# Optimization experiments

Hardware: AMD Instinct MI355X
Metric: run time of the kernel (lower is better)

Reference implementation:

```python
import jax, jax.numpy as jnp
import numpy as np

VOCAB = 32000
E = 512      # embed_dim
H = 512      # hidden_dim (== embed_dim, required by the output-averaging slice)
NUM_LAYERS = 2
WIN = 8
S = 512      # seq_len
B = 8        # batch


def setup_inputs() -> dict:
    key = jax.random.key(0)
    ks = jax.random.split(key, 40)
    d = {"encoder_input": jax.random.randint(ks[0], (S, B), 0, VOCAB, dtype=jnp.int64
                                             if jax.config.jax_enable_x64 else jnp.int32)}
    d["embed_table"] = jax.random.normal(ks[1], (VOCAB, E), jnp.float32) * 0.02
    i = 2
    for l in range(NUM_LAYERS):
        in_dim = E if l == 0 else 2 * H
        for dirn in ("f", "b"):
            sc = 1.0 / np.sqrt(H).astype(np.float32)
            d[f"wih{l}{dirn}"] = jax.random.normal(ks[i], (4 * H, in_dim), jnp.float32) * sc; i += 1
            d[f"whh{l}{dirn}"] = jax.random.normal(ks[i], (4 * H, H), jnp.float32) * sc; i += 1
            d[f"b{l}{dirn}"] = jax.random.normal(ks[i], (4 * H,), jnp.float32) * sc; i += 1
    return d


def _lstm_dir(x, mask, wih, whh, b, reverse):
    """One LSTM direction over padded windows. x: [L, N, in], mask: [L, N, 1].
    Masked (out-of-window) steps carry state unchanged; since invalid steps form a
    prefix in scan order (left pad for fwd, right pad for bwd-reversed), the zero
    initial state is preserved until the first valid step -> identical math to
    running the LSTM on the truncated window, as in the original per-token loop."""
    Hh = whh.shape[1]

    def step(carry, inp):
        h, c = carry
        xt, mt = inp
        g = xt @ wih.T + h @ whh.T + b                      # [N, 4H], torch gate order i,f,g,o
        i_, f_, g_, o_ = jnp.split(g, 4, axis=-1)
        c_new = jax.nn.sigmoid(f_) * c + jax.nn.sigmoid(i_) * jnp.tanh(g_)
        h_new = jax.nn.sigmoid(o_) * jnp.tanh(c_new)
        h = jnp.where(mt, h_new, h)
        c = jnp.where(mt, c_new, c)
        return (h, c), h

    N = x.shape[1]
    h0 = jnp.zeros((N, Hh), x.dtype)
    _, ys = jax.lax.scan(step, (h0, h0), (x, mask), reverse=reverse)
    return ys  # [L, N, Hh]


def _forward(encoder_input, embed_table, layer_params):
    S_, B_ = encoder_input.shape
    L = 2 * WIN + 1
    emb = embed_table[encoder_input]                         # [S, B, E]
    offs = jnp.arange(L) - WIN
    pos = jnp.arange(S_)[:, None] + offs[None, :]            # [S, L]
    valid = (pos >= 0) & (pos < S_)
    pidx = jnp.clip(pos, 0, S_ - 1)
    windows = emb[pidx]                                      # [S, L, B, E]
    x = windows.transpose(1, 0, 2, 3).reshape(L, S_ * B_, E)  # [L, N, E]
    mask = jnp.broadcast_to(valid.T[:, :, None, None], (L, S_, B_, 1)).reshape(L, S_ * B_, 1)
    for (wf, hf, bf, wb, hb, bb) in layer_params:
        yf = _lstm_dir(x, mask, wf, hf, bf, reverse=False)
        yb = _lstm_dir(x, mask, wb, hb, bb, reverse=True)
        x = jnp.concatenate([yf, yb], axis=-1)               # [L, N, 2H]
    out = x[WIN].reshape(S_, B_, 2 * H)                      # [S, B, 2H]
    return (out[:, :, :E] + out[:, :, E:]) / 2


def reference(encoder_input, embed_table,
              wih0f, whh0f, b0f, wih0b, whh0b, b0b,
              wih1f, whh1f, b1f, wih1b, whh1b, b1b):
    layer_params = [(wih0f, whh0f, b0f, wih0b, whh0b, b0b),
                    (wih1f, whh1f, b1f, wih1b, whh1b, b1b)]
    return _forward(encoder_input, embed_table, layer_params)
```

## Files before the change

kernel.cpp:

```cpp
#include <hip/hip_runtime.h>
#include <stdint.h>

typedef __bf16 bf16;
typedef __bf16 bf16x8 __attribute__((ext_vector_type(8)));
typedef __bf16 bf16x4 __attribute__((ext_vector_type(4)));
typedef float f32x4 __attribute__((ext_vector_type(4)));

#define WIN 8

__device__ __forceinline__ float sigm(float x) { return 1.0f / (1.0f + __expf(-x)); }
__device__ __forceinline__ float tanhfast(float x) { return 2.0f / (1.0f + __expf(-2.0f * x)) - 1.0f; }

__device__ __forceinline__ void gload16(const void* g, void* l) {
    __builtin_amdgcn_global_load_lds((const __attribute__((address_space(1))) void*)g,
                                     (__attribute__((address_space(3))) void*)l, 16, 0, 0);
}

struct StepArgs {
    const bf16* A1;
    const bf16* A2;
    const bf16* W;
    const float* bias;
    const bf16* P0;
    float* Cst;
    bf16* Hout;
    float* Hf32;
    const bf16* Hprev;
    int l;
    int firstStep;
};

template<int MODE>
__global__ __launch_bounds__(512, 2)
void step_pair(StepArgs fa, StepArgs ba) {
    const StepArgs a = blockIdx.z ? ba : fa;
    __shared__ alignas(16) char lds[131072];

    constexpr int SA1 = (MODE == 0) ? 512 : 1024;
    constexpr int SW  = (MODE == 2) ? 1536 : 512;
    constexpr int SH  = (MODE == 0) ? 2048 : (MODE == 1 ? 1024 : 512);
    constexpr int SHP = (MODE == 1) ? 1024 : 512;

    const int tid = threadIdx.x;
    const int w = tid >> 6;
    const int lane = tid & 63;
    const int wm = w >> 2, wn = w & 3;
    const int bx = blockIdx.x, by = blockIdx.y;
    const int rowBase = bx * 256;

    int KB;
    if (MODE == 0) KB = 8;
    else if (MODE == 1) KB = a.firstStep ? 0 : 8;
    else KB = a.firstStep ? 16 : 24;

    const int lq = lane >> 3;
    const int lc = lane & 7;
    const int swz = 8 * (lc ^ lq);

    const bf16* aP[4];
    const bf16* a2P[4];
    const bf16* bP[4];
#pragma unroll
    for (int q = 0; q < 4; ++q) {
        const int r = w * 32 + q * 8 + lq;
        const int n = rowBase + r;
        aP[q] = a.A1 ? (a.A1 + (size_t)n * SA1 + swz) : (const bf16*)0;
        if (MODE == 2) a2P[q] = a.A2 ? (a.A2 + (size_t)n * 512 + swz) : (const bf16*)0;
        int wr;
        if (MODE == 0) wr = by * 256 + r;
        else wr = ((r & 63) >> 4) * 512 + by * 64 + (r >> 6) * 16 + (r & 15);
        bP[q] = a.W + (size_t)wr * SW + swz;
    }

    const int l15 = lane & 15, l4 = lane >> 4;
    const int key = (l15 & 7) << 4;
    const int aBase = (wm * 128 + l15) * 128;
    const int bBase = (wn * 64 + l15) * 128;

    f32x4 acc[8][4];
    const f32x4 zf = {0.f, 0.f, 0.f, 0.f};
#pragma unroll
    for (int m = 0; m < 8; ++m)
#pragma unroll
        for (int n = 0; n < 4; ++n) acc[m][n] = zf;

    auto CHUNK = [&](char* Sd, int kb, int q) {
        const int ke = kb * 64;
        const int ldsOff = (w * 32 + q * 8) * 128;
        const bf16* srcA;
        if (MODE == 2) srcA = (kb < 16) ? (aP[q] + ke) : (a2P[q] + (ke - 1024));
        else srcA = aP[q] + ke;
        gload16(srcA, Sd + ldsOff);
        gload16(bP[q] + ke, Sd + 32768 + ldsOff);
    };

    if (KB > 0) {
#pragma unroll
        for (int q = 0; q < 4; ++q) CHUNK(lds, 0, q);
        asm volatile("s_waitcnt vmcnt(0)" ::: "memory");
        __builtin_amdgcn_s_barrier();

        for (int t = 0; t < KB; ++t) {
            const int cur = t & 1;
            const char* Ab = lds + cur * 65536;
            const char* Bb = Ab + 32768;
            char* Sd = lds + (cur ^ 1) * 65536;
            const bool pf = (t + 1 < KB);
            const int ko0 = (l4 * 16) ^ key;
            const int ko1 = (64 + l4 * 16) ^ key;
            bf16x8 af0[4], af1[4], bv0[4], bv1[4];

            if (pf) { CHUNK(Sd, t + 1, 0); CHUNK(Sd, t + 1, 1); }
#pragma unroll
            for (int i = 0; i < 4; ++i)
                af0[i] = *(const bf16x8*)(Ab + aBase + i * 2048 + ko0);
#pragma unroll
            for (int n = 0; n < 4; ++n)
                bv0[n] = *(const bf16x8*)(Bb + bBase + n * 2048 + ko0);
            __builtin_amdgcn_s_barrier();
            asm volatile("s_waitcnt lgkmcnt(0)" ::: "memory");
            __builtin_amdgcn_sched_barrier(0);
            __builtin_amdgcn_s_setprio(1);
#pragma unroll
            for (int i = 0; i < 4; ++i)
#pragma unroll
                for (int n = 0; n < 4; ++n)
                    acc[i][n] = __builtin_amdgcn_mfma_f32_16x16x32_bf16(af0[i], bv0[n], acc[i][n], 0, 0, 0);
            __builtin_amdgcn_s_setprio(0);
            __builtin_amdgcn_sched_barrier(0);
            __builtin_amdgcn_s_barrier();

            if (pf) CHUNK(Sd, t + 1, 2);
#pragma unroll
            for (int i = 0; i < 4; ++i)
                af1[i] = *(const bf16x8*)(Ab + aBase + (4 + i) * 2048 + ko0);
            __builtin_amdgcn_s_barrier();
            asm volatile("s_waitcnt lgkmcnt(0)" ::: "memory");
            __builtin_amdgcn_sched_barrier(0);
            __builtin_amdgcn_s_setprio(1);
#pragma unroll
            for (int i = 0; i < 4; ++i)
#pragma unroll
                for (int n = 0; n < 4; ++n)
                    acc[4 + i][n] = __builtin_amdgcn_mfma_f32_16x16x32_bf16(af1[i], bv0[n], acc[4 + i][n], 0, 0, 0);
            __builtin_amdgcn_s_setprio(0);
            __builtin_amdgcn_sched_barrier(0);
            __builtin_amdgcn_s_barrier();

            if (pf) CHUNK(Sd, t + 1, 3);
#pragma unroll
            for (int i = 0; i < 4; ++i)
                af0[i] = *(const bf16x8*)(Ab + aBase + i * 2048 + ko1);
#pragma unroll
            for (int n = 0; n < 4; ++n)
                bv1[n] = *(const bf16x8*)(Bb + bBase + n * 2048 + ko1);
            __builtin_amdgcn_s_barrier();
            asm volatile("s_waitcnt lgkmcnt(0)" ::: "memory");
            __builtin_amdgcn_sched_barrier(0);
            __builtin_amdgcn_s_setprio(1);
#pragma unroll
            for (int i = 0; i < 4; ++i)
#pragma unroll
                for (int n = 0; n < 4; ++n)
                    acc[i][n] = __builtin_amdgcn_mfma_f32_16x16x32_bf16(af0[i], bv1[n], acc[i][n], 0, 0, 0);
            __builtin_amdgcn_s_setprio(0);
            __builtin_amdgcn_sched_barrier(0);
            __builtin_amdgcn_s_barrier();

#pragma unroll
            for (int i = 0; i < 4; ++i)
                af1[i] = *(const bf16x8*)(Ab + aBase + (4 + i) * 2048 + ko1);
            __builtin_amdgcn_s_barrier();
            asm volatile("s_waitcnt lgkmcnt(0)" ::: "memory");
            __builtin_amdgcn_sched_barrier(0);
            __builtin_amdgcn_s_setprio(1);
#pragma unroll
            for (int i = 0; i < 4; ++i)
#pragma unroll
                for (int n = 0; n < 4; ++n)
                    acc[4 + i][n] = __builtin_amdgcn_mfma_f32_16x16x32_bf16(af1[i], bv1[n], acc[4 + i][n], 0, 0, 0);
            __builtin_amdgcn_s_setprio(0);
            __builtin_amdgcn_sched_barrier(0);
            if (pf) asm volatile("s_waitcnt vmcnt(0)" ::: "memory");
            __builtin_amdgcn_s_barrier();
        }
    }

    if (MODE == 0) {
#pragma unroll
        for (int m = 0; m < 8; ++m)
#pragma unroll
            for (int n = 0; n < 4; ++n) {
                const int col = by * 256 + wn * 64 + n * 16 + l15;
#pragma unroll
                for (int e = 0; e < 4; ++e) {
                    const int row = rowBase + wm * 128 + m * 16 + l4 * 4 + e;
                    a.Hout[(size_t)row * SH + col] = (bf16)acc[m][n][e];
                }
            }
        return;
    }

    const int u = by * 64 + wn * 16 + l15;
    const float bi = a.bias[u];
    const float bff = a.bias[512 + u];
    const float bg = a.bias[1024 + u];
    const float bo = a.bias[1536 + u];
#pragma unroll
    for (int m = 0; m < 8; ++m) {
#pragma unroll
        for (int e = 0; e < 4; ++e) {
            const int n = rowBase + wm * 128 + m * 16 + l4 * 4 + e;
            const int s = n >> 3;
            const int p = s + a.l - WIN;
            const bool valid = ((unsigned)p < 512u);
            float gi = acc[m][0][e] + bi;
            float gf = acc[m][1][e] + bff;
            float gg = acc[m][2][e] + bg;
            float go = acc[m][3][e] + bo;
            if (MODE == 1) {
                const int pc = p < 0 ? 0 : (p > 511 ? 511 : p);
                const size_t pr = (size_t)(pc * 8 + (n & 7)) * 2048;
                gi += (float)a.P0[pr + u];
                gf += (float)a.P0[pr + 512 + u];
                gg += (float)a.P0[pr + 1024 + u];
                go += (float)a.P0[pr + 1536 + u];
            }
            const float cold = a.firstStep ? 0.0f : a.Cst[(size_t)n * 512 + u];
            const float cnew = sigm(gf) * cold + sigm(gi) * tanhfast(gg);
            const float hnew = sigm(go) * tanhfast(cnew);
            float hv, cv;
            if (valid) { hv = hnew; cv = cnew; }
            else {
                hv = a.Hprev ? (float)a.Hprev[(size_t)n * SHP + u] : 0.0f;
                cv = cold;
            }
            a.Cst[(size_t)n * 512 + u] = cv;
            a.Hout[(size_t)n * SH + u] = (bf16)hv;
            if (a.Hf32) a.Hf32[(size_t)n * 512 + u] = hv;
        }
    }
}

__global__ void embed_kernel(const int* __restrict__ tok, const float* __restrict__ tbl,
                             bf16* __restrict__ X0) {
    const int n = blockIdx.x;
    const int t = tok[n];
    const float4 v = ((const float4*)(tbl + (size_t)t * 512))[threadIdx.x];
    bf16x4 o = {(bf16)v.x, (bf16)v.y, (bf16)v.z, (bf16)v.w};
    ((bf16x4*)(X0 + (size_t)n * 512))[threadIdx.x] = o;
}

__global__ void cvt_kernel(const float* __restrict__ src, bf16* __restrict__ dst, int n4) {
    const int i = blockIdx.x * 256 + threadIdx.x;
    if (i < n4) {
        const float4 v = ((const float4*)src)[i];
        bf16x4 o = {(bf16)v.x, (bf16)v.y, (bf16)v.z, (bf16)v.w};
        ((bf16x4*)dst)[i] = o;
    }
}

__global__ void build_w1_kernel(const float* __restrict__ wih, const float* __restrict__ whh,
                                bf16* __restrict__ dst) {
    const int r = blockIdx.x;
    for (int k = threadIdx.x; k < 1536; k += 256) {
        const float v = (k < 1024) ? wih[(size_t)r * 1024 + k] : whh[(size_t)r * 512 + (k - 1024)];
        dst[(size_t)r * 1536 + k] = (bf16)v;
    }
}

__global__ void combine_kernel(const float* __restrict__ hf, const float* __restrict__ hb,
                               float* __restrict__ out) {
    const int i = blockIdx.x * 256 + threadIdx.x;
    const float4 x = ((const float4*)hf)[i];
    const float4 y = ((const float4*)hb)[i];
    float4 r;
    r.x = (x.x + y.x) * 0.5f;
    r.y = (x.y + y.y) * 0.5f;
    r.z = (x.z + y.z) * 0.5f;
    r.w = (x.w + y.w) * 0.5f;
    ((float4*)out)[i] = r;
}

extern "C" void kernel_launch(void* const* d_in, const int* in_sizes, int n_in,
                              void* d_out, int out_size, void* d_ws, size_t ws_size,
                              hipStream_t stream) {
    (void)in_sizes; (void)n_in; (void)out_size;
    const int*   tok   = (const int*)d_in[0];
    const float* tbl   = (const float*)d_in[1];
    const float* wih0f = (const float*)d_in[2];
    const float* whh0f = (const float*)d_in[3];
    const float* b0f   = (const float*)d_in[4];
    const float* wih0b = (const float*)d_in[5];
    const float* whh0b = (const float*)d_in[6];
    const float* b0b   = (const float*)d_in[7];
    const float* wih1f = (const float*)d_in[8];
    const float* whh1f = (const float*)d_in[9];
    const float* b1f   = (const float*)d_in[10];
    const float* wih1b = (const float*)d_in[11];
    const float* whh1b = (const float*)d_in[12];
    const float* b1b   = (const float*)d_in[13];

    char* ws = (char*)d_ws;
    size_t off = 0;
    auto alloc = [&](size_t bytes) -> char* {
        char* p = ws + off;
        off += (bytes + 255) & ~(size_t)255;
        return p;
    };
    bf16* wih0f_b = (bf16*)alloc((size_t)2048 * 512 * 2);
    bf16* wih0b_b = (bf16*)alloc((size_t)2048 * 512 * 2);
    bf16* whh0f_b = (bf16*)alloc((size_t)2048 * 512 * 2);
    bf16* whh0b_b = (bf16*)alloc((size_t)2048 * 512 * 2);
    bf16* w1f_b   = (bf16*)alloc((size_t)2048 * 1536 * 2);
    bf16* w1b_b   = (bf16*)alloc((size_t)2048 * 1536 * 2);
    bf16* X0      = (bf16*)alloc((size_t)4096 * 512 * 2);
    bf16* P0f     = (bf16*)alloc((size_t)4096 * 2048 * 2);
    bf16* P0b     = (bf16*)alloc((size_t)4096 * 2048 * 2);
    bf16* X1      = (bf16*)alloc((size_t)17 * 4096 * 1024 * 2);
    float* c0f    = (float*)alloc((size_t)4096 * 512 * 4);
    float* c0b    = (float*)alloc((size_t)4096 * 512 * 4);
    bf16* h1f0    = (bf16*)alloc((size_t)4096 * 512 * 2);
    bf16* h1f1    = (bf16*)alloc((size_t)4096 * 512 * 2);
    bf16* h1b0    = (bf16*)alloc((size_t)4096 * 512 * 2);
    bf16* h1b1    = (bf16*)alloc((size_t)4096 * 512 * 2);
    float* hf32f  = (float*)alloc((size_t)4096 * 512 * 4);
    float* hf32b  = (float*)alloc((size_t)4096 * 512 * 4);
    if (off > ws_size) return;

    bf16* h1f[2] = {h1f0, h1f1};
    bf16* h1b[2] = {h1b0, h1b1};

    cvt_kernel<<<1024, 256, 0, stream>>>(wih0f, wih0f_b, 262144);
    cvt_kernel<<<1024, 256, 0, stream>>>(wih0b, wih0b_b, 262144);
    cvt_kernel<<<1024, 256, 0, stream>>>(whh0f, whh0f_b, 262144);
    cvt_kernel<<<1024, 256, 0, stream>>>(whh0b, whh0b_b, 262144);
    build_w1_kernel<<<2048, 256, 0, stream>>>(wih1f, whh1f, w1f_b);
    build_w1_kernel<<<2048, 256, 0, stream>>>(wih1b, whh1b, w1b_b);
    embed_kernel<<<4096, 128, 0, stream>>>(tok, tbl, X0);

    dim3 g(16, 8, 2), blk(512, 1, 1);

    {
        StepArgs f{}, b{};
        f.A1 = X0; f.W = wih0f_b; f.Hout = P0f;
        b = f; b.W = wih0b_b; b.Hout = P0b;
        step_pair<0><<<g, blk, 0, stream>>>(f, b);
    }

    const size_t SLOT = (size_t)4096 * 1024;

    for (int i = 0; i <= 16; ++i) {
        const int lf = i, lb = 16 - i;
        StepArgs f{}, b{};
        f.A1 = (lf == 0) ? (const bf16*)0 : X1 + (size_t)(lf - 1) * SLOT;
        f.W = whh0f_b; f.bias = b0f; f.P0 = P0f; f.Cst = c0f;
        f.Hout = X1 + (size_t)lf * SLOT; f.Hprev = f.A1;
        f.l = lf; f.firstStep = (lf == 0) ? 1 : 0;
        b.A1 = (lb == 16) ? (const bf16*)0 : X1 + (size_t)(lb + 1) * SLOT + 512;
        b.W = whh0b_b; b.bias = b0b; b.P0 = P0b; b.Cst = c0b;
        b.Hout = X1 + (size_t)lb * SLOT + 512; b.Hprev = b.A1;
        b.l = lb; b.firstStep = (lb == 16) ? 1 : 0;
        step_pair<1><<<g, blk, 0, stream>>>(f, b);
    }

    for (int i = 0; i <= 8; ++i) {
        const int lf = i, lb = 16 - i;
        StepArgs f{}, b{};
        f.A1 = X1 + (size_t)lf * SLOT;
        f.A2 = (i == 0) ? (const bf16*)0 : h1f[(i + 1) & 1];
        f.W = w1f_b; f.bias = b1f; f.Cst = c0f;
        f.Hout = h1f[i & 1]; f.Hf32 = (i == 8) ? hf32f : (float*)0;
        f.Hprev = f.A2;
        f.l = lf; f.firstStep = (i == 0) ? 1 : 0;
        b.A1 = X1 + (size_t)lb * SLOT;
        b.A2 = (i == 0) ? (const bf16*)0 : h1b[(i + 1) & 1];
        b.W = w1b_b; b.bias = b1b; b.Cst = c0b;
        b.Hout = h1b[i & 1]; b.Hf32 = (i == 8) ? hf32b : (float*)0;
        b.Hprev = b.A2;
        b.l = lb; b.firstStep = (i == 0) ? 1 : 0;
        step_pair<2><<<g, blk, 0, stream>>>(f, b);
    }

    combine_kernel<<<2048, 256, 0, stream>>>(hf32f, hf32b, (float*)d_out);
}
```

Baseline: 1.089 ms.

## Fuse layer-0 input projection into each recurrent step GEMM via concatenated weights

Drops the precomputed layer-0 input projection (P0 GEMM over 4096 tokens) and instead concatenates W_hh and W_ih into one [2048,1024] weight, so each of the 17 layer-0 step kernels does an extra K=512 against shifted embedding rows. This removes the separate projection launch, the P0 buffers, and the scattered bf16 P0 gathers in the epilogue. In exchange it repeats the input projection 17 times, once per window slot, roughly doubling the MFMA work of the layer-0 steps.

```diff
diff --git a/kernel.cpp b/kernel.cpp
--- a/kernel.cpp
+++ b/kernel.cpp
@@ -21,7 +21,6 @@
     const bf16* A2;
     const bf16* W;
     const float* bias;
-    const bf16* P0;
     float* Cst;
     bf16* Hout;
     float* Hf32;
@@ -36,10 +35,12 @@
     const StepArgs a = blockIdx.z ? ba : fa;
     __shared__ alignas(16) char lds[131072];
 
-    constexpr int SA1 = (MODE == 0) ? 512 : 1024;
-    constexpr int SW  = (MODE == 2) ? 1536 : 512;
-    constexpr int SH  = (MODE == 0) ? 2048 : (MODE == 1 ? 1024 : 512);
+    constexpr int SA1 = 1024;
+    constexpr int SA2 = 512;
+    constexpr int SW  = (MODE == 2) ? 1536 : 1024;
+    constexpr int SH  = (MODE == 1) ? 1024 : 512;
     constexpr int SHP = (MODE == 1) ? 1024 : 512;
+    constexpr int ATILES = (MODE == 1) ? 8 : 16;
 
     const int tid = threadIdx.x;
     const int w = tid >> 6;
@@ -48,14 +49,14 @@
     const int bx = blockIdx.x, by = blockIdx.y;
     const int rowBase = bx * 256;
 
-    int KB;
-    if (MODE == 0) KB = 8;
-    else if (MODE == 1) KB = a.firstStep ? 0 : 8;
-    else KB = a.firstStep ? 16 : 24;
+    int KB, kt0;
+    if (MODE == 1) { KB = a.firstStep ? 8 : 16; kt0 = a.firstStep ? 8 : 0; }
+    else           { KB = a.firstStep ? 16 : 24; kt0 = 0; }
 
     const int lq = lane >> 3;
     const int lc = lane & 7;
     const int swz = 8 * (lc ^ lq);
+    const int d = (a.l - WIN) * 8;
 
     const bf16* aP[4];
     const bf16* a2P[4];
@@ -65,10 +66,14 @@
         const int r = w * 32 + q * 8 + lq;
         const int n = rowBase + r;
         aP[q] = a.A1 ? (a.A1 + (size_t)n * SA1 + swz) : (const bf16*)0;
-        if (MODE == 2) a2P[q] = a.A2 ? (a.A2 + (size_t)n * 512 + swz) : (const bf16*)0;
-        int wr;
-        if (MODE == 0) wr = by * 256 + r;
-        else wr = ((r & 63) >> 4) * 512 + by * 64 + (r >> 6) * 16 + (r & 15);
+        if (MODE == 1) {
+            int n2 = n + d;
+            n2 = n2 < 0 ? 0 : (n2 > 4095 ? 4095 : n2);
+            a2P[q] = a.A2 + (size_t)n2 * SA2 + swz;
+        } else {
+            a2P[q] = a.A2 ? (a.A2 + (size_t)n * SA2 + swz) : (const bf16*)0;
+        }
+        const int wr = ((r & 63) >> 4) * 512 + by * 64 + (r >> 6) * 16 + (r & 15);
         bP[q] = a.W + (size_t)wr * SW + swz;
     }
 
@@ -84,19 +89,18 @@
 #pragma unroll
         for (int n = 0; n < 4; ++n) acc[m][n] = zf;
 
-    auto CHUNK = [&](char* Sd, int kb, int q) {
-        const int ke = kb * 64;
+    auto CHUNK = [&](char* Sd, int kt, int q) {
         const int ldsOff = (w * 32 + q * 8) * 128;
         const bf16* srcA;
-        if (MODE == 2) srcA = (kb < 16) ? (aP[q] + ke) : (a2P[q] + (ke - 1024));
-        else srcA = aP[q] + ke;
+        if (kt < ATILES) srcA = aP[q] + kt * 64;
+        else srcA = a2P[q] + (kt - ATILES) * 64;
         gload16(srcA, Sd + ldsOff);
-        gload16(bP[q] + ke, Sd + 32768 + ldsOff);
+        gload16(bP[q] + (size_t)kt * 64, Sd + 32768 + ldsOff);
     };
 
-    if (KB > 0) {
-#pragma unroll
-        for (int q = 0; q < 4; ++q) CHUNK(lds, 0, q);
+    {
+#pragma unroll
+        for (int q = 0; q < 4; ++q) CHUNK(lds, kt0, q);
         asm volatile("s_waitcnt vmcnt(0)" ::: "memory");
         __builtin_amdgcn_s_barrier();
 
@@ -106,11 +110,12 @@
             const char* Bb = Ab + 32768;
             char* Sd = lds + (cur ^ 1) * 65536;
             const bool pf = (t + 1 < KB);
+            const int ktn = t + 1 + kt0;
             const int ko0 = (l4 * 16) ^ key;
             const int ko1 = (64 + l4 * 16) ^ key;
             bf16x8 af0[4], af1[4], bv0[4], bv1[4];
 
-            if (pf) { CHUNK(Sd, t + 1, 0); CHUNK(Sd, t + 1, 1); }
+            if (pf) { CHUNK(Sd, ktn, 0); CHUNK(Sd, ktn, 1); }
 #pragma unroll
             for (int i = 0; i < 4; ++i)
                 af0[i] = *(const bf16x8*)(Ab + aBase + i * 2048 + ko0);
@@ -130,7 +135,7 @@
             __builtin_amdgcn_sched_barrier(0);
             __builtin_amdgcn_s_barrier();
 
-            if (pf) CHUNK(Sd, t + 1, 2);
+            if (pf) CHUNK(Sd, ktn, 2);
 #pragma unroll
             for (int i = 0; i < 4; ++i)
                 af1[i] = *(const bf16x8*)(Ab + aBase + (4 + i) * 2048 + ko0);
@@ -147,7 +152,7 @@
             __builtin_amdgcn_sched_barrier(0);
             __builtin_amdgcn_s_barrier();
 
-            if (pf) CHUNK(Sd, t + 1, 3);
+            if (pf) CHUNK(Sd, ktn, 3);
 #pragma unroll
             for (int i = 0; i < 4; ++i)
                 af0[i] = *(const bf16x8*)(Ab + aBase + i * 2048 + ko1);
@@ -184,21 +189,6 @@
             if (pf) asm volatile("s_waitcnt vmcnt(0)" ::: "memory");
             __builtin_amdgcn_s_barrier();
         }
-    }
-
-    if (MODE == 0) {
-#pragma unroll
-        for (int m = 0; m < 8; ++m)
-#pragma unroll
-            for (int n = 0; n < 4; ++n) {
-                const int col = by * 256 + wn * 64 + n * 16 + l15;
-#pragma unroll
-                for (int e = 0; e < 4; ++e) {
-                    const int row = rowBase + wm * 128 + m * 16 + l4 * 4 + e;
-                    a.Hout[(size_t)row * SH + col] = (bf16)acc[m][n][e];
-                }
-            }
-        return;
     }
 
     const int u = by * 64 + wn * 16 + l15;
@@ -214,18 +204,10 @@
             const int s = n >> 3;
             const int p = s + a.l - WIN;
             const bool valid = ((unsigned)p < 512u);
-            float gi = acc[m][0][e] + bi;
-            float gf = acc[m][1][e] + bff;
-            float gg = acc[m][2][e] + bg;
-            float go = acc[m][3][e] + bo;
-            if (MODE == 1) {
-                const int pc = p < 0 ? 0 : (p > 511 ? 511 : p);
-                const size_t pr = (size_t)(pc * 8 + (n & 7)) * 2048;
-                gi += (float)a.P0[pr + u];
-                gf += (float)a.P0[pr + 512 + u];
-                gg += (float)a.P0[pr + 1024 + u];
-                go += (float)a.P0[pr + 1536 + u];
-            }
+            const float gi = acc[m][0][e] + bi;
+            const float gf = acc[m][1][e] + bff;
+            const float gg = acc[m][2][e] + bg;
+            const float go = acc[m][3][e] + bo;
             const float cold = a.firstStep ? 0.0f : a.Cst[(size_t)n * 512 + u];
             const float cnew = sigm(gf) * cold + sigm(gi) * tanhfast(gg);
             const float hnew = sigm(go) * tanhfast(cnew);
@@ -251,12 +233,12 @@
     ((bf16x4*)(X0 + (size_t)n * 512))[threadIdx.x] = o;
 }
 
-__global__ void cvt_kernel(const float* __restrict__ src, bf16* __restrict__ dst, int n4) {
-    const int i = blockIdx.x * 256 + threadIdx.x;
-    if (i < n4) {
-        const float4 v = ((const float4*)src)[i];
-        bf16x4 o = {(bf16)v.x, (bf16)v.y, (bf16)v.z, (bf16)v.w};
-        ((bf16x4*)dst)[i] = o;
+__global__ void build_w0_kernel(const float* __restrict__ wih, const float* __restrict__ whh,
+                                bf16* __restrict__ dst) {
+    const int r = blockIdx.x;
+    for (int k = threadIdx.x; k < 1024; k += 256) {
+        const float v = (k < 512) ? whh[(size_t)r * 512 + k] : wih[(size_t)r * 512 + (k - 512)];
+        dst[(size_t)r * 1024 + k] = (bf16)v;
     }
 }
 
@@ -308,15 +290,11 @@
         off += (bytes + 255) & ~(size_t)255;
         return p;
     };
-    bf16* wih0f_b = (bf16*)alloc((size_t)2048 * 512 * 2);
-    bf16* wih0b_b = (bf16*)alloc((size_t)2048 * 512 * 2);
-    bf16* whh0f_b = (bf16*)alloc((size_t)2048 * 512 * 2);
-    bf16* whh0b_b = (bf16*)alloc((size_t)2048 * 512 * 2);
+    bf16* w0f_b   = (bf16*)alloc((size_t)2048 * 1024 * 2);
+    bf16* w0b_b   = (bf16*)alloc((size_t)2048 * 1024 * 2);
     bf16* w1f_b   = (bf16*)alloc((size_t)2048 * 1536 * 2);
     bf16* w1b_b   = (bf16*)alloc((size_t)2048 * 1536 * 2);
     bf16* X0      = (bf16*)alloc((size_t)4096 * 512 * 2);
-    bf16* P0f     = (bf16*)alloc((size_t)4096 * 2048 * 2);
-    bf16* P0b     = (bf16*)alloc((size_t)4096 * 2048 * 2);
     bf16* X1      = (bf16*)alloc((size_t)17 * 4096 * 1024 * 2);
     float* c0f    = (float*)alloc((size_t)4096 * 512 * 4);
     float* c0b    = (float*)alloc((size_t)4096 * 512 * 4);
@@ -331,34 +309,26 @@
     bf16* h1f[2] = {h1f0, h1f1};
     bf16* h1b[2] = {h1b0, h1b1};
 
-    cvt_kernel<<<1024, 256, 0, stream>>>(wih0f, wih0f_b, 262144);
-    cvt_kernel<<<1024, 256, 0, stream>>>(wih0b, wih0b_b, 262144);
-    cvt_kernel<<<1024, 256, 0, stream>>>(whh0f, whh0f_b, 262144);
-    cvt_kernel<<<1024, 256, 0, stream>>>(whh0b, whh0b_b, 262144);
+    build_w0_kernel<<<2048, 256, 0, stream>>>(wih0f, whh0f, w0f_b);
+    build_w0_kernel<<<2048, 256, 0, stream>>>(wih0b, whh0b, w0b_b);
     build_w1_kernel<<<2048, 256, 0, stream>>>(wih1f, whh1f, w1f_b);
     build_w1_kernel<<<2048, 256, 0, stream>>>(wih1b, whh1b, w1b_b);
     embed_kernel<<<4096, 128, 0, stream>>>(tok, tbl, X0);
 
     dim3 g(16, 8, 2), blk(512, 1, 1);
-
-    {
-        StepArgs f{}, b{};
-        f.A1 = X0; f.W = wih0f_b; f.Hout = P0f;
-        b = f; b.W = wih0b_b; b.Hout = P0b;
-        step_pair<0><<<g, blk, 0, stream>>>(f, b);
-    }
-
     const size_t SLOT = (size_t)4096 * 1024;
 
     for (int i = 0; i <= 16; ++i) {
         const int lf = i, lb = 16 - i;
         StepArgs f{}, b{};
         f.A1 = (lf == 0) ? (const bf16*)0 : X1 + (size_t)(lf - 1) * SLOT;
-        f.W = whh0f_b; f.bias = b0f; f.P0 = P0f; f.Cst = c0f;
+        f.A2 = X0;
+        f.W = w0f_b; f.bias = b0f; f.Cst = c0f;
         f.Hout = X1 + (size_t)lf * SLOT; f.Hprev = f.A1;
         f.l = lf; f.firstStep = (lf == 0) ? 1 : 0;
         b.A1 = (lb == 16) ? (const bf16*)0 : X1 + (size_t)(lb + 1) * SLOT + 512;
-        b.W = whh0b_b; b.bias = b0b; b.P0 = P0b; b.Cst = c0b;
+        b.A2 = X0;
+        b.W = w0b_b; b.bias = b0b; b.Cst = c0b;
         b.Hout = X1 + (size_t)lb * SLOT + 512; b.Hprev = b.A1;
         b.l = lb; b.firstStep = (lb == 16) ? 1 : 0;
         step_pair<1><<<g, blk, 0, stream>>>(f, b);
```

After: 1.266 ms. 1.16x slower.

## Software-pipeline LDS fragment loads one phase ahead of MFMA in GEMM loop

Applied to the files above, without the earlier changes.

Restructures the inner K-loop so the LDS fragment reads for the next MFMA phase are issued before the current phase's MFMAs. Partial lgkmcnt waits replace full drains, so LDS reads overlap matrix math. The first fragments of the next K-block are preloaded from the freshly filled buffer at the end of each iteration. This adds register pressure from extra live fragment arrays, and it relies on the hand-counted lgkmcnt values being correct.

```diff
diff --git a/kernel.cpp b/kernel.cpp
--- a/kernel.cpp
+++ b/kernel.cpp
@@ -95,10 +95,20 @@
     };
 
     if (KB > 0) {
+        const int ko0 = (l4 * 16) ^ key;
+        const int ko1 = (64 + l4 * 16) ^ key;
+        bf16x8 afA[4], afB[4], bv0[4], bvp[4];
+
 #pragma unroll
         for (int q = 0; q < 4; ++q) CHUNK(lds, 0, q);
         asm volatile("s_waitcnt vmcnt(0)" ::: "memory");
         __builtin_amdgcn_s_barrier();
+#pragma unroll
+        for (int i = 0; i < 4; ++i)
+            afA[i] = *(const bf16x8*)(lds + aBase + i * 2048 + ko0);
+#pragma unroll
+        for (int n = 0; n < 4; ++n)
+            bv0[n] = *(const bf16x8*)(lds + 32768 + bBase + n * 2048 + ko0);
 
         for (int t = 0; t < KB; ++t) {
             const int cur = t & 1;
@@ -106,82 +116,82 @@
             const char* Bb = Ab + 32768;
             char* Sd = lds + (cur ^ 1) * 65536;
             const bool pf = (t + 1 < KB);
-            const int ko0 = (l4 * 16) ^ key;
-            const int ko1 = (64 + l4 * 16) ^ key;
-            bf16x8 af0[4], af1[4], bv0[4], bv1[4];
 
             if (pf) { CHUNK(Sd, t + 1, 0); CHUNK(Sd, t + 1, 1); }
 #pragma unroll
             for (int i = 0; i < 4; ++i)
-                af0[i] = *(const bf16x8*)(Ab + aBase + i * 2048 + ko0);
+                afB[i] = *(const bf16x8*)(Ab + aBase + (4 + i) * 2048 + ko0);
+            __builtin_amdgcn_s_barrier();
+            asm volatile("s_waitcnt lgkmcnt(4)" ::: "memory");
+            __builtin_amdgcn_sched_barrier(0);
+            __builtin_amdgcn_s_setprio(1);
+#pragma unroll
+            for (int i = 0; i < 4; ++i)
+#pragma unroll
+                for (int n = 0; n < 4; ++n)
+                    acc[i][n] = __builtin_amdgcn_mfma_f32_16x16x32_bf16(afA[i], bv0[n], acc[i][n], 0, 0, 0);
+            __builtin_amdgcn_s_setprio(0);
+            __builtin_amdgcn_sched_barrier(0);
+            __builtin_amdgcn_s_barrier();
+
+            if (pf) { CHUNK(Sd, t + 1, 2); CHUNK(Sd, t + 1, 3); }
+#pragma unroll
+            for (int i = 0; i < 4; ++i)
+                afA[i] = *(const bf16x8*)(Ab + aBase + i * 2048 + ko1);
 #pragma unroll
             for (int n = 0; n < 4; ++n)
-                bv0[n] = *(const bf16x8*)(Bb + bBase + n * 2048 + ko0);
-            __builtin_amdgcn_s_barrier();
-            asm volatile("s_waitcnt lgkmcnt(0)" ::: "memory");
+                bvp[n] = *(const bf16x8*)(Bb + bBase + n * 2048 + ko1);
+            __builtin_amdgcn_s_barrier();
+            asm volatile("s_waitcnt lgkmcnt(8)" ::: "memory");
             __builtin_amdgcn_sched_barrier(0);
             __builtin_amdgcn_s_setprio(1);
 #pragma unroll
             for (int i = 0; i < 4; ++i)
 #pragma unroll
                 for (int n = 0; n < 4; ++n)
-                    acc[i][n] = __builtin_amdgcn_mfma_f32_16x16x32_bf16(af0[i], bv0[n], acc[i][n], 0, 0, 0);
+                    acc[4 + i][n] = __builtin_amdgcn_mfma_f32_16x16x32_bf16(afB[i], bv0[n], acc[4 + i][n], 0, 0, 0);
             __builtin_amdgcn_s_setprio(0);
             __builtin_amdgcn_sched_barrier(0);
             __builtin_amdgcn_s_barrier();
 
-            if (pf) CHUNK(Sd, t + 1, 2);
-#pragma unroll
-            for (int i = 0; i < 4; ++i)
-                af1[i] = *(const bf16x8*)(Ab + aBase + (4 + i) * 2048 + ko0);
-            __builtin_amdgcn_s_barrier();
-            asm volatile("s_waitcnt lgkmcnt(0)" ::: "memory");
+#pragma unroll
+            for (int i = 0; i < 4; ++i)
+                afB[i] = *(const bf16x8*)(Ab + aBase + (4 + i) * 2048 + ko1);
+            __builtin_amdgcn_s_barrier();
+            asm volatile("s_waitcnt lgkmcnt(4)" ::: "memory");
             __builtin_amdgcn_sched_barrier(0);
             __builtin_amdgcn_s_setprio(1);
 #pragma unroll
             for (int i = 0; i < 4; ++i)
 #pragma unroll
                 for (int n = 0; n < 4; ++n)
-                    acc[4 + i][n] = __builtin_amdgcn_mfma_f32_16x16x32_bf16(af1[i], bv0[n], acc[4 + i][n], 0, 0, 0);
+                    acc[i][n] = __builtin_amdgcn_mfma_f32_16x16x32_bf16(afA[i], bvp[n], acc[i][n], 0, 0, 0);
             __builtin_amdgcn_s_setprio(0);
             __builtin_amdgcn_sched_barrier(0);
             __builtin_amdgcn_s_barrier();
 
-            if (pf) CHUNK(Sd, t + 1, 3);
-#pragma unroll
-            for (int i = 0; i < 4; ++i)
-                af0[i] = *(const bf16x8*)(Ab + aBase + i * 2048 + ko1);
-#pragma unroll
-            for (int n = 0; n < 4; ++n)
-                bv1[n] = *(const bf16x8*)(Bb + bBase + n * 2048 + ko1);
-            __builtin_amdgcn_s_barrier();
-            asm volatile("s_waitcnt lgkmcnt(0)" ::: "memory");
+            if (pf) asm volatile("s_waitcnt vmcnt(0)" ::: "memory");
+            __builtin_amdgcn_s_barrier();
+            if (pf) {
+#pragma unroll
+                for (int i = 0; i < 4; ++i)
+                    afA[i] = *(const bf16x8*)(Sd + aBase + i * 2048 + ko0);
+#pragma unroll
+                for (int n = 0; n < 4; ++n)
+                    bv0[n] = *(const bf16x8*)(Sd + 32768 + bBase + n * 2048 + ko0);
+                asm volatile("s_waitcnt lgkmcnt(8)" ::: "memory");
+            } else {
+                asm volatile("s_waitcnt lgkmcnt(0)" ::: "memory");
+            }
             __builtin_amdgcn_sched_barrier(0);
             __builtin_amdgcn_s_setprio(1);
 #pragma unroll
             for (int i = 0; i < 4; ++i)
 #pragma unroll
                 for (int n = 0; n < 4; ++n)
-                    acc[i][n] = __builtin_amdgcn_mfma_f32_16x16x32_bf16(af0[i], bv1[n], acc[i][n], 0, 0, 0);
+                    acc[4 + i][n] = __builtin_amdgcn_mfma_f32_16x16x32_bf16(afB[i], bvp[n], acc[4 + i][n], 0, 0, 0);
             __builtin_amdgcn_s_setprio(0);
             __builtin_amdgcn_sched_barrier(0);
-            __builtin_amdgcn_s_barrier();
-
-#pragma unroll
-            for (int i = 0; i < 4; ++i)
-                af1[i] = *(const bf16x8*)(Ab + aBase + (4 + i) * 2048 + ko1);
-            __builtin_amdgcn_s_barrier();
-            asm volatile("s_waitcnt lgkmcnt(0)" ::: "memory");
-            __builtin_amdgcn_sched_barrier(0);
-            __builtin_amdgcn_s_setprio(1);
-#pragma unroll
-            for (int i = 0; i < 4; ++i)
-#pragma unroll
-                for (int n = 0; n < 4; ++n)
-                    acc[4 + i][n] = __builtin_amdgcn_mfma_f32_16x16x32_bf16(af1[i], bv1[n], acc[4 + i][n], 0, 0, 0);
-            __builtin_amdgcn_s_setprio(0);
-            __builtin_amdgcn_sched_barrier(0);
-            if (pf) asm volatile("s_waitcnt vmcnt(0)" ::: "memory");
             __builtin_amdgcn_s_barrier();
         }
     }
```

Result: no change. 1.104 ms (+1.4%).
